# Performance work log

Hardware: AMD Instinct MI355X
Metric: run time of the kernel (lower is better)

The kernel has to match this reference:

```python
import jax, jax.numpy as jnp
import numpy as np

EPS_LN = 1e-6  # ieps_ln_default


def setup_inputs() -> dict:
    key = jax.random.key(0)
    ks = jax.random.split(key, 8)
    B, S, H, ID = 8, 2048, 8, 256  # batch, seq, heads, i_head_dim
    OD = 256                        # o_head_dim
    sc_hid = 1.0 / np.sqrt(2 * ID)
    sc_og = 1.0 / np.sqrt(ID + OD)
    return {
        "heads_input": jax.random.normal(ks[0], (B, S, H, ID), dtype=jnp.float32),
        "W_hid": jax.random.uniform(ks[1], (3 * OD, 2 * ID), jnp.float32, -sc_hid, sc_hid),
        "b_hid": jnp.zeros((3 * OD,), jnp.float32),
        "W_og": jax.random.uniform(ks[2], (OD, ID + OD), jnp.float32, -sc_og, sc_og),
        "b_og": jnp.zeros((OD,), jnp.float32),
        "ln_w": jnp.ones((H, ID), jnp.float32),
        "ln_b": jnp.zeros((H, ID), jnp.float32),
        "init_cx": jnp.zeros((H, OD), jnp.float32),
    }


def _forward(heads_input, W_hid, b_hid, W_og, b_og, ln_w, ln_b, init_cx):
    B, S, H, ID = heads_input.shape
    OD = init_cx.shape[-1]
    # RS1cumsumstatnorm: causal running sum, LayerNorm over (heads, dim) jointly
    csum = jnp.cumsum(heads_input, axis=1)
    mean = jnp.mean(csum, axis=(-2, -1), keepdims=True)
    var = jnp.var(csum, axis=(-2, -1), keepdims=True)
    csum = (csum - mean) * jax.lax.rsqrt(var + EPS_LN) * ln_w + ln_b
    # trans_hid on cat(input, csum): [B,S,H,2*ID] -> [B,S,H,3*OD]
    x2 = jnp.concatenate([heads_input, csum], axis=-1)
    g = jnp.einsum('bshd,od->bsho', x2, W_hid) + b_hid
    g = g.reshape(B, S, H, 3, OD)
    igate, fgate, hidden = g[..., 0, :], g[..., 1, :], g[..., 2, :]
    fgate = jax.nn.sigmoid(fgate)
    igh = jax.nn.sigmoid(igate) * jax.nn.relu(hidden)
    # LGateFunc: cell_t = f_t * cell_{t-1} + igh_t, starting from init_cx
    c0 = jnp.broadcast_to(init_cx, (B, H, OD))

    def step(c, fi):
        f, ig = fi
        c = f * c + ig
        return c, c

    _, cells = jax.lax.scan(step, c0, (jnp.moveaxis(fgate, 1, 0), jnp.moveaxis(igh, 1, 0)))
    cell = jnp.moveaxis(cells, 0, 1)  # [B,S,H,OD]
    # output gate on cat(input, cell)
    xo = jnp.concatenate([heads_input, cell], axis=-1)
    og = jax.nn.sigmoid(jnp.einsum('bshd,od->bsho', xo, W_og) + b_og)
    return og * cell


def reference(heads_input, W_hid, b_hid, W_og, b_og, ln_w, ln_b, init_cx):
    return _forward(heads_input, W_hid, b_hid, W_og, b_og, ln_w, ln_b, init_cx)
```

## Files before the change

### kernel.cpp

```cpp
#include <hip/hip_runtime.h>

typedef unsigned short u16;
typedef unsigned int u32;

typedef __attribute__((ext_vector_type(8))) short bf16x8;
typedef __attribute__((ext_vector_type(4))) float f32x4;

#define B_ 8
#define S_ 2048
#define H_ 8
#define ID_ 256
#define OD_ 256
#define K_ 512
#define M_ (B_*S_*H_)
#define N1_ 768
#define N2_ 256
#define G2_ 512

#define CSCH 64
#define CSST (S_/CSCH)

#define OFF_X2   (0ull)
#define SZ_X2    ((unsigned long long)M_*K_*2)
#define OFF_G    (OFF_X2 + SZ_X2)
#define SZ_G     ((unsigned long long)M_*G2_*2)
#define OFF_WH   (OFF_G + SZ_G)
#define SZ_WH    ((unsigned long long)N1_*K_*2)
#define OFF_WO   (OFF_WH + SZ_WH)
#define SZ_WO    ((unsigned long long)N2_*K_*2)
#define OFF_AUX  (OFF_WO + SZ_WO)
#define SZ_AUX   ((unsigned long long)B_*CSCH*2048*4)
#define OFF_CF   (OFF_AUX + SZ_AUX)
#define SZ_CARR  ((unsigned long long)B_*H_*32*256*4)
#define OFF_CC   (OFF_CF + SZ_CARR)
#define OFF_CIN  (OFF_CC + SZ_CARR)

__device__ __forceinline__ u16 f2bf(float f) {
    union { float f; u32 u; } v; v.f = f;
    u32 u = v.u;
    u += 0x7fffu + ((u >> 16) & 1u);
    return (u16)(u >> 16);
}
__device__ __forceinline__ float bf2f(u16 h) {
    union { u32 u; float f; } v; v.u = ((u32)h) << 16;
    return v.f;
}
__device__ __forceinline__ u32 pack2h(float a, float b) {
    union { _Float16 h; u16 u; } x, y;
    x.h = (_Float16)a; y.h = (_Float16)b;
    return (u32)x.u | ((u32)y.u << 16);
}
__device__ __forceinline__ float h2f(u16 u) {
    union { u16 u; _Float16 h; } v; v.u = u;
    return (float)v.h;
}
__device__ __forceinline__ float sigm(float x) {
    return 1.0f / (1.0f + __expf(-x));
}

__device__ __forceinline__ void gld16(const void* g, void* l) {
    __builtin_amdgcn_global_load_lds(
        (const __attribute__((address_space(1))) void*)g,
        (__attribute__((address_space(3))) void*)l, 16, 0, 0);
}

__device__ __forceinline__ int whid_src_row(int n) {
    const int t = n >> 8, c = n & 255;
    if (t < 2) {
        const int wn = c >> 6, jj = (c >> 4) & 3, l = c & 15;
        const int o = t * 128 + wn * 32 + (jj & 1) * 16 + l;
        return (jj < 2) ? o : (512 + o);
    }
    return 256 + (n - 512);
}

__global__ __launch_bounds__(256) void wconv_kernel(
    const float* __restrict__ Whid, const float* __restrict__ Wog,
    u16* __restrict__ WhB, u16* __restrict__ WoB)
{
    int idx = blockIdx.x * 256 + threadIdx.x;
    if (idx < N1_*K_) {
        const int n = idx >> 9, k = idx & 511;
        WhB[idx] = f2bf(Whid[(size_t)whid_src_row(n) * K_ + k]);
    }
    if (idx < N2_*K_) WoB[idx] = f2bf(Wog[idx]);
}

__global__ __launch_bounds__(256) void csum_phase1(
    const float* __restrict__ X, float* __restrict__ aux)
{
    const int bch = blockIdx.x;
    const int b = bch / CSCH, ch = bch % CSCH;
    const int t = threadIdx.x;
    float acc[8];
#pragma unroll
    for (int h = 0; h < 8; ++h) acc[h] = 0.f;
    for (int i = 0; i < CSST; ++i) {
        const int s = ch * CSST + i;
        const float* xp = X + ((size_t)(b * S_ + s)) * 2048 + t;
#pragma unroll
        for (int h = 0; h < 8; ++h) acc[h] += xp[h * 256];
    }
    float* ap = aux + (size_t)bch * 2048 + t;
#pragma unroll
    for (int h = 0; h < 8; ++h) ap[h * 256] = acc[h];
}

__global__ __launch_bounds__(256) void csum_mid(float* __restrict__ aux)
{
    const int idx = blockIdx.x * 256 + threadIdx.x;
    const int b = idx >> 11, c = idx & 2047;
    float run = 0.f;
    for (int ch = 0; ch < CSCH; ++ch) {
        float* p = aux + ((size_t)(b * CSCH + ch)) * 2048 + c;
        float v = *p; *p = run; run += v;
    }
}

__global__ __launch_bounds__(256) void csum_phase2(
    const float* __restrict__ X, const float* __restrict__ aux,
    const float* __restrict__ lnw, const float* __restrict__ lnb,
    u16* __restrict__ x2)
{
    const int bch = blockIdx.x;
    const int b = bch / CSCH, ch = bch % CSCH;
    const int t = threadIdx.x;
    float c[8], wv[8], bv[8];
#pragma unroll
    for (int h = 0; h < 8; ++h) {
        c[h]  = aux[(size_t)bch * 2048 + h * 256 + t];
        wv[h] = lnw[h * 256 + t];
        bv[h] = lnb[h * 256 + t];
    }
    __shared__ float red[2][4];
    for (int i = 0; i < CSST; ++i) {
        const int s = ch * CSST + i;
        const float* xp = X + ((size_t)(b * S_ + s)) * 2048 + t;
        float xa[8];
#pragma unroll
        for (int h = 0; h < 8; ++h) { xa[h] = xp[h * 256]; c[h] += xa[h]; }
        float sx = 0.f, sq = 0.f;
#pragma unroll
        for (int h = 0; h < 8; ++h) { sx += c[h]; sq += c[h] * c[h]; }
#pragma unroll
        for (int off = 32; off >= 1; off >>= 1) {
            sx += __shfl_down(sx, (unsigned)off);
            sq += __shfl_down(sq, (unsigned)off);
        }
        const int wid = t >> 6;
        if ((t & 63) == 0) { red[0][wid] = sx; red[1][wid] = sq; }
        __syncthreads();
        const float tsx = red[0][0] + red[0][1] + red[0][2] + red[0][3];
        const float tsq = red[1][0] + red[1][1] + red[1][2] + red[1][3];
        __syncthreads();
        const float mean = tsx * (1.f / 2048.f);
        const float var  = tsq * (1.f / 2048.f) - mean * mean;
        const float rstd = rsqrtf(var + 1e-6f);
        const size_t mrow = ((size_t)(b * S_ + s)) * H_;
#pragma unroll
        for (int h = 0; h < 8; ++h) {
            u16* row = x2 + (mrow + h) * (size_t)K_;
            row[t]       = f2bf(xa[h]);
            row[256 + t] = f2bf((c[h] - mean) * rstd * wv[h] + bv[h]);
        }
    }
}

template<int N, int EPI>
__global__ __launch_bounds__(512, 2) void gemm_kernel(
    const u16* __restrict__ A, const u16* __restrict__ Bw,
    u16* __restrict__ Gout, const float* __restrict__ bias,
    const u16* __restrict__ cellbuf, float* __restrict__ Out)
{
    constexpr int NT = N / 256;
    constexpr int KT = K_ / 32;
    const int blk = blockIdx.x;
    const int xcd = blk & 7;
    const int j = blk >> 3;
    const int tileN = j % NT;
    const int tileM = (j / NT) * 8 + xcd;
    const int m0 = tileM * 256, n0 = tileN * 256;
    const int tid = threadIdx.x;
    const int lane = tid & 63;
    const int w = tid >> 6;
    const int wm = w >> 2, wn = w & 3;
    const int l15 = lane & 15, quad = lane >> 4;

    __shared__ __align__(16) u16 smem[4 * 16384];

    const int srow   = lane >> 2;
    const int schunk = ((lane & 3) ^ ((lane >> 3) & 3)) * 8;
    const u16* gA0 = A  + (size_t)(m0 + w * 32      + srow) * K_ + schunk;
    const u16* gA1 = A  + (size_t)(m0 + w * 32 + 16 + srow) * K_ + schunk;
    const u16* gB0 = Bw + (size_t)(n0 + w * 32      + srow) * K_ + schunk;
    const u16* gB1 = Bw + (size_t)(n0 + w * 32 + 16 + srow) * K_ + schunk;

    auto STAGE = [&](int bufb, int kt) {
        u16* sb = smem + bufb * 16384;
        gld16(gA0 + kt * 32, sb + (w * 32) * 32);
        gld16(gA1 + kt * 32, sb + (w * 32 + 16) * 32);
        gld16(gB0 + kt * 32, sb + 8192 + (w * 32) * 32);
        gld16(gB1 + kt * 32, sb + 8192 + (w * 32 + 16) * 32);
    };

    const int swz  = (quad ^ ((l15 >> 1) & 3)) * 8;
    const int aoff = (wm * 128 + l15) * 32 + swz;
    const int boff = 8192 + (wn * 64 + l15) * 32 + swz;

    f32x4 acc[8][4];
    const f32x4 zero4 = {0.f, 0.f, 0.f, 0.f};
#pragma unroll
    for (int mi = 0; mi < 8; ++mi)
#pragma unroll
        for (int jj = 0; jj < 4; ++jj) acc[mi][jj] = zero4;

    STAGE(0, 0); STAGE(1, 1); STAGE(2, 2);
    asm volatile("s_waitcnt vmcnt(8)\n\ts_barrier" ::: "memory");

#pragma unroll
    for (int kt = 0; kt < KT; ++kt) {
        const int cur = kt & 3;
        if (kt + 3 < KT) STAGE((kt + 3) & 3, kt + 3);
        const u16* sb = smem + cur * 16384;
        bf16x8 af[8], bfr[4];
#pragma unroll
        for (int mi = 0; mi < 8; ++mi)
            af[mi] = *(const bf16x8*)(const void*)(&sb[aoff + mi * 512]);
#pragma unroll
        for (int jj = 0; jj < 4; ++jj)
            bfr[jj] = *(const bf16x8*)(const void*)(&sb[boff + jj * 512]);
        __builtin_amdgcn_s_setprio(1);
#pragma unroll
        for (int mi = 0; mi < 8; ++mi)
#pragma unroll
            for (int jj = 0; jj < 4; ++jj)
                acc[mi][jj] = __builtin_amdgcn_mfma_f32_16x16x32_bf16(
                    af[mi], bfr[jj], acc[mi][jj], 0, 0, 0);
        __builtin_amdgcn_s_setprio(0);
        if (kt + 1 < KT) {
            if (kt + 3 < KT)
                asm volatile("s_waitcnt vmcnt(8) lgkmcnt(0)\n\ts_barrier" ::: "memory");
            else if (kt + 2 < KT)
                asm volatile("s_waitcnt vmcnt(4) lgkmcnt(0)\n\ts_barrier" ::: "memory");
            else
                asm volatile("s_waitcnt vmcnt(0) lgkmcnt(0)\n\ts_barrier" ::: "memory");
        }
    }

    const int m_base = m0 + wm * 128 + quad * 4;
    if (EPI == 0) {
        if (tileN < 2) {
            const int o0 = tileN * 128 + wn * 32 + l15;
            const float bI0 = bias[o0],            bI1 = bias[o0 + 16];
            const float bH0 = bias[512 + o0],      bH1 = bias[512 + o0 + 16];
            const int q = (tileN * 4 + wn) * 16 + l15;
#pragma unroll
            for (int mi = 0; mi < 8; ++mi) {
#pragma unroll
                for (int r = 0; r < 4; ++r) {
                    const int m = m_base + mi * 16 + r;
                    const float ig0 = sigm(acc[mi][0][r] + bI0) * fmaxf(acc[mi][2][r] + bH0, 0.f);
                    const float ig1 = sigm(acc[mi][1][r] + bI1) * fmaxf(acc[mi][3][r] + bH1, 0.f);
                    *(u32*)(void*)(Gout + (size_t)m * G2_ + 2 * q) = pack2h(ig0, ig1);
                }
            }
        } else {
            const int o0 = wn * 64 + l15;
            const float bF0 = bias[256 + o0],       bF1 = bias[256 + o0 + 16];
            const float bF2 = bias[256 + o0 + 32],  bF3 = bias[256 + o0 + 48];
            const int qA = wn * 32 + l15, qB = qA + 16;
#pragma unroll
            for (int mi = 0; mi < 8; ++mi) {
#pragma unroll
                for (int r = 0; r < 4; ++r) {
                    const int m = m_base + mi * 16 + r;
                    u16* row = Gout + (size_t)m * G2_ + 256;
                    *(u32*)(void*)(row + 2 * qA) =
                        pack2h(sigm(acc[mi][0][r] + bF0), sigm(acc[mi][1][r] + bF1));
                    *(u32*)(void*)(row + 2 * qB) =
                        pack2h(sigm(acc[mi][2][r] + bF2), sigm(acc[mi][3][r] + bF3));
                }
            }
        }
    } else {
        const int colb = wn * 64 + l15;
        float bb[4];
#pragma unroll
        for (int jj = 0; jj < 4; ++jj) bb[jj] = bias[colb + jj * 16];
#pragma unroll
        for (int mi = 0; mi < 8; ++mi) {
#pragma unroll
            for (int r = 0; r < 4; ++r) {
                const int m = m_base + mi * 16 + r;
                const u16* cp = cellbuf + (size_t)m * K_ + 256 + colb;
                float* op = Out + (size_t)m * N2_ + colb;
#pragma unroll
                for (int jj = 0; jj < 4; ++jj)
                    op[jj * 16] = sigm(acc[mi][jj][r] + bb[jj]) * bf2f(cp[jj * 16]);
            }
        }
    }
}

__global__ __launch_bounds__(256) void scan_phase1(
    const u16* __restrict__ g2, float* __restrict__ cF, float* __restrict__ cC)
{
    const int blk = blockIdx.x;
    const int chp = blk & 7, bh = blk >> 3;
    const int h = bh & 7, b = bh >> 3;
    const int t = threadIdx.x;
    const int ch = chp * 4 + (t >> 6);
    const int o = (t & 63) * 4;
    float F[4] = {1.f, 1.f, 1.f, 1.f};
    float c[4] = {0.f, 0.f, 0.f, 0.f};
    for (int i = 0; i < 64; ++i) {
        const int s = ch * 64 + i;
        const size_t m = ((size_t)(b * S_ + s)) * H_ + h;
        const u16* gp = g2 + m * G2_;
        const uint2 igp = *(const uint2*)(const void*)(gp + o);
        const uint2 fgp = *(const uint2*)(const void*)(gp + 256 + o);
        const float f0 = h2f((u16)fgp.x), f1 = h2f((u16)(fgp.x >> 16));
        const float f2 = h2f((u16)fgp.y), f3 = h2f((u16)(fgp.y >> 16));
        c[0] = f0 * c[0] + h2f((u16)igp.x);         F[0] *= f0;
        c[1] = f1 * c[1] + h2f((u16)(igp.x >> 16)); F[1] *= f1;
        c[2] = f2 * c[2] + h2f((u16)igp.y);         F[2] *= f2;
        c[3] = f3 * c[3] + h2f((u16)(igp.y >> 16)); F[3] *= f3;
    }
    const size_t idx = ((size_t)(bh * 32 + ch)) * 256 + o;
    *(float4*)(void*)(cF + idx) = make_float4(F[0], F[1], F[2], F[3]);
    *(float4*)(void*)(cC + idx) = make_float4(c[0], c[1], c[2], c[3]);
}

__global__ __launch_bounds__(256) void scan_mid(
    const float* __restrict__ cF, const float* __restrict__ cC,
    const float* __restrict__ initcx, float* __restrict__ cin)
{
    const int bh = blockIdx.x;
    const int h = bh & 7;
    const int a = threadIdx.x;
    const int q = a >> 1, hfl = a & 1;
    const int ro = ((q >> 4) << 5) + (q & 15) + (hfl << 4);
    float c = initcx[h * 256 + ro];
    for (int ch = 0; ch < 32; ++ch) {
        const size_t idx = ((size_t)(bh * 32 + ch)) * 256 + a;
        cin[idx] = c;
        c = cF[idx] * c + cC[idx];
    }
}

__global__ __launch_bounds__(256) void scan_phase2(
    const u16* __restrict__ g2, const float* __restrict__ cin,
    u16* __restrict__ x2)
{
    const int blk = blockIdx.x;
    const int chp = blk & 7, bh = blk >> 3;
    const int h = bh & 7, b = bh >> 3;
    const int t = threadIdx.x;
    const int ch = chp * 4 + (t >> 6);
    const int z = t & 63;
    const int o = z * 4;
    const int oA = ((z >> 3) << 5) + ((z & 7) << 1);
    const size_t idx = ((size_t)(bh * 32 + ch)) * 256 + o;
    float4 c4 = *(const float4*)(const void*)(cin + idx);
    float c[4] = {c4.x, c4.y, c4.z, c4.w};
    for (int i = 0; i < 64; ++i) {
        const int s = ch * 64 + i;
        const size_t m = ((size_t)(b * S_ + s)) * H_ + h;
        const u16* gp = g2 + m * G2_;
        const uint2 igp = *(const uint2*)(const void*)(gp + o);
        const uint2 fgp = *(const uint2*)(const void*)(gp + 256 + o);
        const float f0 = h2f((u16)fgp.x), f1 = h2f((u16)(fgp.x >> 16));
        const float f2 = h2f((u16)fgp.y), f3 = h2f((u16)(fgp.y >> 16));
        c[0] = f0 * c[0] + h2f((u16)igp.x);
        c[1] = f1 * c[1] + h2f((u16)(igp.x >> 16));
        c[2] = f2 * c[2] + h2f((u16)igp.y);
        c[3] = f3 * c[3] + h2f((u16)(igp.y >> 16));
        u16* xr = x2 + m * K_ + 256;
        const u32 pkA = (u32)f2bf(c[0]) | ((u32)f2bf(c[2]) << 16);
        const u32 pkB = (u32)f2bf(c[1]) | ((u32)f2bf(c[3]) << 16);
        *(u32*)(void*)(xr + oA)      = pkA;
        *(u32*)(void*)(xr + oA + 16) = pkB;
    }
}

extern "C" void kernel_launch(void* const* d_in, const int* in_sizes, int n_in,
                              void* d_out, int out_size, void* d_ws, size_t ws_size,
                              hipStream_t stream)
{
    const float* X      = (const float*)d_in[0];
    const float* Whid   = (const float*)d_in[1];
    const float* bhid   = (const float*)d_in[2];
    const float* Wog    = (const float*)d_in[3];
    const float* bog    = (const float*)d_in[4];
    const float* lnw    = (const float*)d_in[5];
    const float* lnb    = (const float*)d_in[6];
    const float* initcx = (const float*)d_in[7];
    float* out = (float*)d_out;

    char* ws = (char*)d_ws;
    u16* x2   = (u16*)(ws + OFF_X2);
    u16* g    = (u16*)(ws + OFF_G);
    u16* WhB  = (u16*)(ws + OFF_WH);
    u16* WoB  = (u16*)(ws + OFF_WO);
    float* aux = (float*)(ws + OFF_AUX);
    float* cF  = (float*)(ws + OFF_CF);
    float* cC  = (float*)(ws + OFF_CC);
    float* cin = (float*)(ws + OFF_CIN);

    wconv_kernel<<<(N1_*K_ + 255) / 256, 256, 0, stream>>>(Whid, Wog, WhB, WoB);
    csum_phase1<<<B_ * CSCH, 256, 0, stream>>>(X, aux);
    csum_mid<<<64, 256, 0, stream>>>(aux);
    csum_phase2<<<B_ * CSCH, 256, 0, stream>>>(X, aux, lnw, lnb, x2);
    gemm_kernel<N1_, 0><<<(M_ / 256) * (N1_ / 256), 512, 0, stream>>>(
        x2, WhB, g, bhid, nullptr, nullptr);
    scan_phase1<<<B_ * H_ * 8, 256, 0, stream>>>(g, cF, cC);
    scan_mid<<<B_ * H_, 256, 0, stream>>>(cF, cC, initcx, cin);
    scan_phase2<<<B_ * H_ * 8, 256, 0, stream>>>(g, cin, x2);
    gemm_kernel<N2_, 1><<<(M_ / 256) * (N2_ / 256), 512, 0, stream>>>(
        x2, WoB, nullptr, bog, x2, out);
}
```

Measured before the change: 562.3 us.

## Split GEMM k-step into two phases interleaving global loads with MFMA halves

The GEMM main loop now runs each k-tile in two halves. Each half issues part of the next-stage global-to-LDS load (A first, then B) and reads half of the A fragments, then runs 16 MFMAs, with s_barrier and sched_barrier fencing between the phases. The aim is to spread memory issue across the compute and keep the matrix cores busy, in the style of ping-pong scheduling. The cost is more barriers per iteration, and the staging-buffer reuse must still be race-free.

```diff
diff --git a/kernel.cpp b/kernel.cpp
--- a/kernel.cpp
+++ b/kernel.cpp
@@ -195,10 +195,13 @@
     const u16* gB0 = Bw + (size_t)(n0 + w * 32      + srow) * K_ + schunk;
     const u16* gB1 = Bw + (size_t)(n0 + w * 32 + 16 + srow) * K_ + schunk;
 
-    auto STAGE = [&](int bufb, int kt) {
+    auto STAGE_A = [&](int bufb, int kt) {
         u16* sb = smem + bufb * 16384;
         gld16(gA0 + kt * 32, sb + (w * 32) * 32);
         gld16(gA1 + kt * 32, sb + (w * 32 + 16) * 32);
+    };
+    auto STAGE_B = [&](int bufb, int kt) {
+        u16* sb = smem + bufb * 16384;
         gld16(gB0 + kt * 32, sb + 8192 + (w * 32) * 32);
         gld16(gB1 + kt * 32, sb + 8192 + (w * 32 + 16) * 32);
     };
@@ -214,36 +217,60 @@
 #pragma unroll
         for (int jj = 0; jj < 4; ++jj) acc[mi][jj] = zero4;
 
-    STAGE(0, 0); STAGE(1, 1); STAGE(2, 2);
+    STAGE_A(0, 0); STAGE_B(0, 0);
+    STAGE_A(1, 1); STAGE_B(1, 1);
+    STAGE_A(2, 2); STAGE_B(2, 2);
     asm volatile("s_waitcnt vmcnt(8)\n\ts_barrier" ::: "memory");
 
 #pragma unroll
     for (int kt = 0; kt < KT; ++kt) {
         const int cur = kt & 3;
-        if (kt + 3 < KT) STAGE((kt + 3) & 3, kt + 3);
         const u16* sb = smem + cur * 16384;
-        bf16x8 af[8], bfr[4];
-#pragma unroll
-        for (int mi = 0; mi < 8; ++mi)
-            af[mi] = *(const bf16x8*)(const void*)(&sb[aoff + mi * 512]);
+        bf16x8 af0[4], af1[4], bfr[4];
+
 #pragma unroll
         for (int jj = 0; jj < 4; ++jj)
             bfr[jj] = *(const bf16x8*)(const void*)(&sb[boff + jj * 512]);
+#pragma unroll
+        for (int mi = 0; mi < 4; ++mi)
+            af0[mi] = *(const bf16x8*)(const void*)(&sb[aoff + mi * 512]);
+        if (kt + 3 < KT) STAGE_A((kt + 3) & 3, kt + 3);
+        asm volatile("s_barrier" ::: "memory");
+        asm volatile("s_waitcnt lgkmcnt(0)" ::: "memory");
+        __builtin_amdgcn_sched_barrier(0);
         __builtin_amdgcn_s_setprio(1);
 #pragma unroll
-        for (int mi = 0; mi < 8; ++mi)
+        for (int mi = 0; mi < 4; ++mi)
 #pragma unroll
             for (int jj = 0; jj < 4; ++jj)
                 acc[mi][jj] = __builtin_amdgcn_mfma_f32_16x16x32_bf16(
-                    af[mi], bfr[jj], acc[mi][jj], 0, 0, 0);
+                    af0[mi], bfr[jj], acc[mi][jj], 0, 0, 0);
         __builtin_amdgcn_s_setprio(0);
+        asm volatile("s_barrier" ::: "memory");
+
+#pragma unroll
+        for (int mi = 0; mi < 4; ++mi)
+            af1[mi] = *(const bf16x8*)(const void*)(&sb[aoff + (mi + 4) * 512]);
+        if (kt + 3 < KT) STAGE_B((kt + 3) & 3, kt + 3);
+        asm volatile("s_barrier" ::: "memory");
+        asm volatile("s_waitcnt lgkmcnt(0)" ::: "memory");
+        __builtin_amdgcn_sched_barrier(0);
+        __builtin_amdgcn_s_setprio(1);
+#pragma unroll
+        for (int mi = 0; mi < 4; ++mi)
+#pragma unroll
+            for (int jj = 0; jj < 4; ++jj)
+                acc[mi + 4][jj] = __builtin_amdgcn_mfma_f32_16x16x32_bf16(
+                    af1[mi], bfr[jj], acc[mi + 4][jj], 0, 0, 0);
+        __builtin_amdgcn_s_setprio(0);
+
         if (kt + 1 < KT) {
             if (kt + 3 < KT)
-                asm volatile("s_waitcnt vmcnt(8) lgkmcnt(0)\n\ts_barrier" ::: "memory");
+                asm volatile("s_waitcnt vmcnt(8)\n\ts_barrier" ::: "memory");
             else if (kt + 2 < KT)
-                asm volatile("s_waitcnt vmcnt(4) lgkmcnt(0)\n\ts_barrier" ::: "memory");
+                asm volatile("s_waitcnt vmcnt(4)\n\ts_barrier" ::: "memory");
             else
-                asm volatile("s_waitcnt vmcnt(0) lgkmcnt(0)\n\ts_barrier" ::: "memory");
+                asm volatile("s_waitcnt vmcnt(0)\n\ts_barrier" ::: "memory");
         }
     }
 
```

Measured after the change: 557.1 us. No clear change (-0.9%).
